# Kernel tuning notes

Measured on AMD Instinct MI355X. Metric: run time of the kernel, lower is better.

## Reference

```python
import jax, jax.numpy as jnp
import numpy as np

D_MODEL = 1024

def setup_inputs() -> dict:
    key = jax.random.key(0)
    kx, kq, kk, kv, ko = jax.random.split(key, 5)
    x = jax.random.normal(kx, (4, 4096, D_MODEL), dtype=jnp.float32)
    w_q = jax.random.normal(kq, (D_MODEL, D_MODEL), dtype=jnp.float32)
    w_k = jax.random.normal(kk, (D_MODEL, D_MODEL), dtype=jnp.float32)
    w_v = jax.random.normal(kv, (D_MODEL, D_MODEL), dtype=jnp.float32)
    w_o = jax.random.normal(ko, (D_MODEL, D_MODEL), dtype=jnp.float32)
    return {"x": x, "w_q": w_q, "w_k": w_k, "w_v": w_v, "w_o": w_o}

def reference(x, w_q, w_k, w_v, w_o):
    # Q/K/V projections: [B,T,D] @ [D,D] -> [B,T,D]
    q = jnp.einsum('btd,de->bte', x, w_q)
    k = jnp.einsum('btd,de->bte', x, w_k)
    v = jnp.einsum('btd,de->bte', x, w_v)
    # Unnormalized attention: scores [B,T,T] (no softmax)
    scores = jnp.einsum('btd,bsd->bts', q, k)
    attn_output = jnp.einsum('bts,bsd->btd', scores, v)
    # Output projection
    output = jnp.einsum('btd,de->bte', attn_output, w_o)
    return output
```

## Files before the change

### kernel.cpp

```cpp
#include <hip/hip_runtime.h>
#include <hip/hip_bf16.h>
#include <stdint.h>

typedef unsigned short u16;
typedef short bf16x8 __attribute__((ext_vector_type(8)));
typedef float f32x4 __attribute__((ext_vector_type(4)));

#define GLOAD16(gp, lp) __builtin_amdgcn_global_load_lds( \
    (const __attribute__((address_space(1))) uint32_t*)(gp), \
    (__attribute__((address_space(3))) uint32_t*)(lp), 16, 0, 0)

#define VMCNT10 do { asm volatile("s_waitcnt vmcnt(10)" ::: "memory"); \
                     __builtin_amdgcn_sched_barrier(0); } while (0)
#define SBAR    do { __builtin_amdgcn_s_barrier(); \
                     __builtin_amdgcn_sched_barrier(0); } while (0)
#define LGKM0   do { asm volatile("s_waitcnt lgkmcnt(0)" ::: "memory"); \
                     __builtin_amdgcn_sched_barrier(0); } while (0)

__device__ __forceinline__ u16 f2bf(float f) {
  union { float f; uint32_t u; } x; x.f = f;
  return (u16)((x.u + 0x7FFFu + ((x.u >> 16) & 1u)) >> 16);
}
__device__ __forceinline__ float bf2f(u16 h) {
  union { uint32_t u; float f; } x; x.u = (uint32_t)h << 16;
  return x.f;
}

__device__ __forceinline__ void xcd_swizzle(int& bx, int& by, int& bz) {
  const int gx = gridDim.x, gy = gridDim.y;
  const int nwg = gx * gy * (int)gridDim.z;
  const int lin = ((int)blockIdx.z * gy + (int)blockIdx.y) * gx + (int)blockIdx.x;
  const int q = nwg >> 3;
  const int wl = (lin & 7) * q + (lin >> 3);
  bz = wl / (gx * gy);
  const int rem = wl - bz * gx * gy;
  by = rem / gx;
  bx = rem - by * gx;
}

__global__ __launch_bounds__(256) void cast_stream(const float* __restrict__ x,
                                                   const float* __restrict__ wq,
                                                   const float* __restrict__ wk,
                                                   const float* __restrict__ wv,
                                                   const float* __restrict__ wo,
                                                   u16* __restrict__ xb,
                                                   u16* __restrict__ WA,
                                                   u16* __restrict__ WBb) {
  __shared__ float tile[64][65];
  const int lin = blockIdx.x;
  const int t = threadIdx.x;
  if (lin < 2048) {
    const float* src = x + (size_t)lin * 8192;
    u16* dst = xb + (size_t)lin * 8192;
#pragma unroll
    for (int i = 0; i < 4; ++i) {
      const int e = i * 2048 + t * 8;
      float4 a = *(const float4*)&src[e];
      float4 b = *(const float4*)&src[e + 4];
      u16 p[8];
      p[0] = f2bf(a.x); p[1] = f2bf(a.y); p[2] = f2bf(a.z); p[3] = f2bf(a.w);
      p[4] = f2bf(b.x); p[5] = f2bf(b.y); p[6] = f2bf(b.z); p[7] = f2bf(b.w);
      *(uint4*)&dst[e] = *(const uint4*)p;
    }
  } else if (lin < 3584) {
    const int e0 = (lin - 2048) * 2048 + t * 8;
    const int w = e0 >> 20;
    const int loc = e0 & 1048575;
    const float* in = w == 0 ? wq : w == 1 ? wk : wv;
    u16* o = w == 0 ? WA : w == 1 ? WBb : WBb + 1048576;
    float4 a = *(const float4*)&in[loc];
    float4 b = *(const float4*)&in[loc + 4];
    u16 p[8];
    p[0] = f2bf(a.x); p[1] = f2bf(a.y); p[2] = f2bf(a.z); p[3] = f2bf(a.w);
    p[4] = f2bf(b.x); p[5] = f2bf(b.y); p[6] = f2bf(b.z); p[7] = f2bf(b.w);
    *(uint4*)&o[loc] = *(const uint4*)p;
  } else {
    const int w2 = lin - 3584;
    const int r0 = (w2 >> 4) * 64, c0 = (w2 & 15) * 64;
    const int lr = t >> 2, lc = (t & 3) * 16;
    const float* src = wo + (size_t)(r0 + lr) * 1024 + c0 + lc;
#pragma unroll
    for (int j = 0; j < 4; ++j) {
      float4 v = *(const float4*)&src[j * 4];
      tile[lr][lc + j * 4 + 0] = v.x;
      tile[lr][lc + j * 4 + 1] = v.y;
      tile[lr][lc + j * 4 + 2] = v.z;
      tile[lr][lc + j * 4 + 3] = v.w;
    }
    __syncthreads();
    u16 tr[16];
#pragma unroll
    for (int j = 0; j < 16; ++j) tr[j] = f2bf(tile[lc + j][lr]);
    u16* dst = WA + 1048576 + (size_t)(c0 + lr) * 1024 + r0 + lc;
    *(uint4*)&dst[0] = *(const uint4*)&tr[0];
    *(uint4*)&dst[8] = *(const uint4*)&tr[8];
  }
}

__global__ __launch_bounds__(256) void transpose_x(const u16* __restrict__ xb,
                                                   u16* __restrict__ xTt) {
  __shared__ u16 ldsT[128][72];
  const int tile = blockIdx.x;
  const int dtile = tile >> 8, tchunk = tile & 255;
  const int t = threadIdx.x;
  const int lr = t >> 2;
  const int dq = (t & 3) * 32;
  const u16* src = xb + (size_t)(tchunk * 64 + lr) * 1024 + dtile * 128 + dq;
#pragma unroll
  for (int i = 0; i < 4; ++i) {
    u16 v[8];
    *(uint4*)v = *(const uint4*)&src[i * 8];
#pragma unroll
    for (int j = 0; j < 8; ++j) ldsT[dq + i * 8 + j][lr] = v[j];
  }
  __syncthreads();
  const int d = t >> 1, seg = (t & 1) * 32;
  u16* dst = xTt + (size_t)tile * 8192 + d * 64 + seg;
#pragma unroll
  for (int i = 0; i < 4; ++i)
    *(uint4*)&dst[i * 8] = *(const uint4*)&ldsT[d][seg + i * 8];
}

__global__ __launch_bounds__(512) void gram_w12(const u16* __restrict__ xTt,
                                                u16* __restrict__ Gp,
                                                const u16* __restrict__ WA,
                                                const u16* __restrict__ WBb,
                                                u16* __restrict__ W12) {
  __shared__ u16 lds[2 * 8192];
  const int lin = blockIdx.x;
  const int wl = (lin & 7) * 88 + (lin >> 3);
  const u16 *Abase, *Bbase;
  u16* Cb;
  int lda, sKt, ldc;
  if (wl < 576) {
    const int z = wl / 36, t5 = wl - z * 36;
    const int b = z >> 2, kc = z & 3;
    int ti = 0;
    while ((ti + 1) * (ti + 2) / 2 <= t5) ++ti;
    const int tj = t5 - ti * (ti + 1) / 2;
    const int tc0 = b * 64 + kc * 16;
    Abase = xTt + (size_t)(ti * 256 + tc0) * 8192;
    Bbase = xTt + (size_t)(tj * 256 + tc0) * 8192;
    lda = 64; sKt = 8192;
    Cb = Gp + ((size_t)z * 36 + t5) * 16384;
    ldc = 128;
  } else {
    const int w = wl - 576;
    const int z2 = w >> 6, tl = w & 63;
    const int by = tl >> 3, bx = tl & 7;
    Abase = WA + (size_t)z2 * 1048576 + (size_t)(by * 128) * 1024;
    Bbase = WBb + (size_t)z2 * 1048576 + (size_t)(bx * 128) * 1024;
    lda = 1024; sKt = 64;
    Cb = W12 + (size_t)z2 * 1048576 + (size_t)(by * 128) * 1024 + bx * 128;
    ldc = 1024;
  }

  const int t = threadIdx.x;
  const int l = t & 63;
  const int wid = t >> 6;
  const int wr = wid >> 2, wc = wid & 3;
  const int lr16 = l & 15, hi = l >> 4;

  f32x4 acc[4][2];
#pragma unroll
  for (int m = 0; m < 4; ++m)
#pragma unroll
    for (int n = 0; n < 2; ++n) acc[m][n] = (f32x4){0.f, 0.f, 0.f, 0.f};

  for (int s = 0; s < 16; ++s) {
    __syncthreads();
    const u16* As = Abase + (size_t)s * sKt;
    const u16* Bs = Bbase + (size_t)s * sKt;
#pragma unroll
    for (int i = 0; i < 2; ++i) {
      int slot = i * 512 + t;
      int row = slot >> 3, cp = slot & 7;
      int clog = cp ^ (row & 7);
      GLOAD16(As + (size_t)row * lda + clog * 8, &lds[slot * 8]);
    }
#pragma unroll
    for (int i = 0; i < 2; ++i) {
      int slot = i * 512 + t;
      int row = slot >> 3, cp = slot & 7;
      int clog = cp ^ (row & 7);
      GLOAD16(Bs + (size_t)row * lda + clog * 8, &lds[8192 + slot * 8]);
    }
    asm volatile("s_waitcnt vmcnt(0)" ::: "memory");
    __syncthreads();
#pragma unroll
    for (int ks = 0; ks < 2; ++ks) {
      bf16x8 af[4], bfr[2];
#pragma unroll
      for (int m = 0; m < 4; ++m) {
        int row = wr * 64 + m * 16 + lr16;
        int p = (ks * 4 + hi) ^ (row & 7);
        af[m] = *(const bf16x8*)&lds[row * 64 + p * 8];
      }
#pragma unroll
      for (int n = 0; n < 2; ++n) {
        int row = wc * 32 + n * 16 + lr16;
        int p = (ks * 4 + hi) ^ (row & 7);
        bfr[n] = *(const bf16x8*)&lds[8192 + row * 64 + p * 8];
      }
#pragma unroll
      for (int m = 0; m < 4; ++m)
#pragma unroll
        for (int n = 0; n < 2; ++n)
          acc[m][n] = __builtin_amdgcn_mfma_f32_16x16x32_bf16(af[m], bfr[n], acc[m][n], 0, 0, 0);
    }
  }

#pragma unroll
  for (int m = 0; m < 4; ++m) {
    int row0 = wr * 64 + m * 16 + hi * 4;
#pragma unroll
    for (int n = 0; n < 2; ++n) {
      int col = wc * 32 + n * 16 + lr16;
      f32x4 v = acc[m][n];
#pragma unroll
      for (int r = 0; r < 4; ++r) Cb[(size_t)(row0 + r) * ldc + col] = f2bf(v[r]);
    }
  }
}

__global__ __launch_bounds__(512) void gemm_bt8(const u16* __restrict__ A,
                                                const u16* __restrict__ B,
                                                u16* __restrict__ C,
                                                int lda, int ldb, int ldc, int K,
                                                size_t sA, size_t sB, size_t sC) {
  __shared__ u16 lds[2 * 8192];
  int bx, by, bz;
  xcd_swizzle(bx, by, bz);
  A += (size_t)bz * sA;
  B += (size_t)bz * sB;
  const int t = threadIdx.x;
  const int l = t & 63;
  const int wid = t >> 6;
  const int wr = wid >> 2, wc = wid & 3;
  const int lr16 = l & 15, hi = l >> 4;
  const int mBase = by * 128;
  const int nBase = bx * 128;

  f32x4 acc[4][2];
#pragma unroll
  for (int m = 0; m < 4; ++m)
#pragma unroll
    for (int n = 0; n < 2; ++n) acc[m][n] = (f32x4){0.f, 0.f, 0.f, 0.f};

  for (int kt = 0; kt < K; kt += 64) {
    __syncthreads();
#pragma unroll
    for (int i = 0; i < 2; ++i) {
      int s = i * 512 + t;
      int row = s >> 3, cp = s & 7;
      int clog = cp ^ (row & 7);
      GLOAD16(A + (size_t)(mBase + row) * lda + kt + clog * 8, &lds[s * 8]);
    }
#pragma unroll
    for (int i = 0; i < 2; ++i) {
      int s = i * 512 + t;
      int row = s >> 3, cp = s & 7;
      int clog = cp ^ (row & 7);
      GLOAD16(B + (size_t)(nBase + row) * ldb + kt + clog * 8, &lds[8192 + s * 8]);
    }
    asm volatile("s_waitcnt vmcnt(0)" ::: "memory");
    __syncthreads();
#pragma unroll
    for (int ks = 0; ks < 2; ++ks) {
      bf16x8 af[4], bfr[2];
#pragma unroll
      for (int m = 0; m < 4; ++m) {
        int row = wr * 64 + m * 16 + lr16;
        int p = (ks * 4 + hi) ^ (row & 7);
        af[m] = *(const bf16x8*)&lds[row * 64 + p * 8];
      }
#pragma unroll
      for (int n = 0; n < 2; ++n) {
        int row = wc * 32 + n * 16 + lr16;
        int p = (ks * 4 + hi) ^ (row & 7);
        bfr[n] = *(const bf16x8*)&lds[8192 + row * 64 + p * 8];
      }
#pragma unroll
      for (int m = 0; m < 4; ++m)
#pragma unroll
        for (int n = 0; n < 2; ++n)
          acc[m][n] = __builtin_amdgcn_mfma_f32_16x16x32_bf16(af[m], bfr[n], acc[m][n], 0, 0, 0);
    }
  }

#pragma unroll
  for (int m = 0; m < 4; ++m) {
    int row0 = mBase + wr * 64 + m * 16 + hi * 4;
#pragma unroll
    for (int n = 0; n < 2; ++n) {
      int col = nBase + wc * 32 + n * 16 + lr16;
      f32x4 v = acc[m][n];
      u16* Cb = C + (size_t)bz * sC;
#pragma unroll
      for (int r = 0; r < 4; ++r) Cb[(size_t)(row0 + r) * ldc + col] = f2bf(v[r]);
    }
  }
}

__global__ __launch_bounds__(256) void reduce_mirror(const u16* __restrict__ Gp,
                                                     u16* __restrict__ G) {
  __shared__ u16 ldsT[128][136];
  const int t5 = blockIdx.x;
  const int b = blockIdx.y;
  int ti = 0;
  while ((ti + 1) * (ti + 2) / 2 <= t5) ++ti;
  const int tj = t5 - ti * (ti + 1) / 2;
  const int tid = threadIdx.x;
  const int rr = tid >> 4, ccc = (tid & 15) * 8;
  u16* Gb = G + (size_t)b * 1048576;
  const size_t ZS = (size_t)36 * 16384;
  const u16* base = Gp + ((size_t)(b * 4) * 36 + t5) * 16384;
#pragma unroll
  for (int i = 0; i < 8; ++i) {
    int row = i * 16 + rr;
    const u16* p = base + row * 128 + ccc;
    u16 a0[8], a1[8], a2[8], a3[8], o[8];
    *(uint4*)a0 = *(const uint4*)&p[0];
    *(uint4*)a1 = *(const uint4*)&p[ZS];
    *(uint4*)a2 = *(const uint4*)&p[2 * ZS];
    *(uint4*)a3 = *(const uint4*)&p[3 * ZS];
#pragma unroll
    for (int j = 0; j < 8; ++j)
      o[j] = f2bf(bf2f(a0[j]) + bf2f(a1[j]) + bf2f(a2[j]) + bf2f(a3[j]));
    *(uint4*)&Gb[(size_t)(ti * 128 + row) * 1024 + tj * 128 + ccc] = *(const uint4*)o;
    *(uint4*)&ldsT[row][ccc] = *(const uint4*)o;
  }
  if (ti != tj) {
    __syncthreads();
#pragma unroll
    for (int i = 0; i < 8; ++i) {
      int row = i * 16 + rr;
      u16 m8[8];
#pragma unroll
      for (int j = 0; j < 8; ++j) m8[j] = ldsT[ccc + j][row];
      *(uint4*)&Gb[(size_t)(tj * 128 + row) * 1024 + ti * 128 + ccc] = *(const uint4*)m8;
    }
  }
}

template <bool F32OUT>
__device__ __forceinline__ void gemm256_core(const u16* __restrict__ A,
                                             const u16* __restrict__ B,
                                             void* __restrict__ C,
                                             int lda, int ldb, int ldc, int K,
                                             int mBase, int nBase, u16* lds) {
  const int t = threadIdx.x;
  const int l = t & 63;
  const int wid = t >> 6;
  const int wr = wid >> 2;
  const int wc = wid & 3;
  const int lr16 = l & 15, hi = l >> 4;
  const int rl0 = t >> 3;
  const int rl1 = rl0 + 64;
  const int cp  = t & 7;
  const int cs  = cp ^ (rl0 & 7);
  const int NT = K >> 6;

  f32x4 acc[8][4];
#pragma unroll
  for (int m = 0; m < 8; ++m)
#pragma unroll
    for (int n = 0; n < 4; ++n) acc[m][n] = (f32x4){0.f, 0.f, 0.f, 0.f};

  auto stage = [&](const u16* g0, int ld, u16* d) {
    GLOAD16(g0 + (size_t)rl0 * ld + cs * 8, d + rl0 * 64 + cp * 8);
    GLOAD16(g0 + (size_t)rl1 * ld + cs * 8, d + rl1 * 64 + cp * 8);
  };
  stage(A + (size_t)mBase * lda,          lda, lds + 0);
  stage(B + (size_t)nBase * ldb,          ldb, lds + 16384);
  stage(B + (size_t)(nBase + 128) * ldb,  ldb, lds + 24576);
  stage(A + (size_t)(mBase + 128) * lda,  lda, lds + 8192);
  stage(B + (size_t)nBase * ldb + 64,         ldb, lds + 32768 + 16384);
  stage(A + (size_t)mBase * lda + 64,         lda, lds + 32768);
  stage(B + (size_t)(nBase + 128) * ldb + 64, ldb, lds + 32768 + 24576);

  bf16x8 af[4][2], b0[2][2], b1[2][2];

  for (int tt = 0; tt < NT; ++tt) {
    const int cur = tt & 1;
    u16* bufA = lds + cur * 32768;
    u16* bufB = bufA + 16384;
    u16* bufN = lds + ((tt + 1) & 1) * 32768;
    int t1 = tt + 1; if (t1 >= NT) t1 -= NT;
    int t2 = tt + 2; if (t2 >= NT) t2 -= NT;
    const int k1 = t1 * 64, k2 = t2 * 64;

    VMCNT10;
    SBAR;
    stage(A + (size_t)(mBase + 128) * lda + k1, lda, bufN + 8192);
#pragma unroll
    for (int mi = 0; mi < 4; ++mi) {
      int row = wr * 64 + mi * 16 + lr16;
#pragma unroll
      for (int kk = 0; kk < 2; ++kk) {
        int p = (kk * 4 + hi) ^ (row & 7);
        af[mi][kk] = *(const bf16x8*)&bufA[row * 64 + p * 8];
      }
    }
#pragma unroll
    for (int ni = 0; ni < 2; ++ni) {
      int row = wc * 32 + ni * 16 + lr16;
#pragma unroll
      for (int kk = 0; kk < 2; ++kk) {
        int p = (kk * 4 + hi) ^ (row & 7);
        b0[ni][kk] = *(const bf16x8*)&bufB[row * 64 + p * 8];
      }
    }
    LGKM0;
    __builtin_amdgcn_s_setprio(1);
#pragma unroll
    for (int kk = 0; kk < 2; ++kk)
#pragma unroll
      for (int mi = 0; mi < 4; ++mi)
#pragma unroll
        for (int ni = 0; ni < 2; ++ni)
          acc[mi][ni] = __builtin_amdgcn_mfma_f32_16x16x32_bf16(af[mi][kk], b0[ni][kk], acc[mi][ni], 0, 0, 0);
    __builtin_amdgcn_s_setprio(0);

    VMCNT10;
    SBAR;
    stage(B + (size_t)nBase * ldb + k2, ldb, bufB);
#pragma unroll
    for (int ni = 0; ni < 2; ++ni) {
      int row = 128 + wc * 32 + ni * 16 + lr16;
#pragma unroll
      for (int kk = 0; kk < 2; ++kk) {
        int p = (kk * 4 + hi) ^ (row & 7);
        b1[ni][kk] = *(const bf16x8*)&bufB[row * 64 + p * 8];
      }
    }
    LGKM0;
    __builtin_amdgcn_s_setprio(1);
#pragma unroll
    for (int kk = 0; kk < 2; ++kk)
#pragma unroll
      for (int mi = 0; mi < 4; ++mi)
#pragma unroll
        for (int ni = 0; ni < 2; ++ni)
          acc[mi][2 + ni] = __builtin_amdgcn_mfma_f32_16x16x32_bf16(af[mi][kk], b1[ni][kk], acc[mi][2 + ni], 0, 0, 0);
    __builtin_amdgcn_s_setprio(0);

    VMCNT10;
    SBAR;
    stage(A + (size_t)mBase * lda + k2, lda, bufA);
#pragma unroll
    for (int mi = 0; mi < 4; ++mi) {
      int row = 128 + wr * 64 + mi * 16 + lr16;
#pragma unroll
      for (int kk = 0; kk < 2; ++kk) {
        int p = (kk * 4 + hi) ^ (row & 7);
        af[mi][kk] = *(const bf16x8*)&bufA[row * 64 + p * 8];
      }
    }
    LGKM0;
    __builtin_amdgcn_s_setprio(1);
#pragma unroll
    for (int kk = 0; kk < 2; ++kk)
#pragma unroll
      for (int mi = 0; mi < 4; ++mi)
#pragma unroll
        for (int ni = 0; ni < 2; ++ni)
          acc[4 + mi][2 + ni] = __builtin_amdgcn_mfma_f32_16x16x32_bf16(af[mi][kk], b1[ni][kk], acc[4 + mi][2 + ni], 0, 0, 0);
    __builtin_amdgcn_s_setprio(0);

    SBAR;
    stage(B + (size_t)(nBase + 128) * ldb + k2, ldb, bufB + 8192);
    __builtin_amdgcn_s_setprio(1);
#pragma unroll
    for (int kk = 0; kk < 2; ++kk)
#pragma unroll
      for (int mi = 0; mi < 4; ++mi)
#pragma unroll
        for (int ni = 0; ni < 2; ++ni)
          acc[4 + mi][ni] = __builtin_amdgcn_mfma_f32_16x16x32_bf16(af[mi][kk], b0[ni][kk], acc[4 + mi][ni], 0, 0, 0);
    __builtin_amdgcn_s_setprio(0);
  }

#pragma unroll
  for (int m = 0; m < 8; ++m) {
    int row0 = mBase + (m >> 2) * 128 + wr * 64 + (m & 3) * 16 + hi * 4;
#pragma unroll
    for (int n = 0; n < 4; ++n) {
      int col = nBase + (n >> 1) * 128 + wc * 32 + (n & 1) * 16 + lr16;
      f32x4 v = acc[m][n];
      if (F32OUT) {
        float* Cf = (float*)C;
#pragma unroll
        for (int r = 0; r < 4; ++r) Cf[(size_t)(row0 + r) * ldc + col] = v[r];
      } else {
        u16* Cb = (u16*)C;
#pragma unroll
        for (int r = 0; r < 4; ++r) Cb[(size_t)(row0 + r) * ldc + col] = f2bf(v[r]);
      }
    }
  }
}

__global__ __launch_bounds__(512) void gemm256_out(const u16* __restrict__ xb,
                                                   const u16* __restrict__ PT,
                                                   float* __restrict__ out) {
  __shared__ u16 lds[65536];
  int bx, by, bz;
  xcd_swizzle(bx, by, bz);
  const u16* Bp = PT + (size_t)(by >> 4) * 1048576;
  gemm256_core<true>(xb, Bp, out, 1024, 1024, 1024, 1024, by * 256, bx * 256, lds);
}

extern "C" void kernel_launch(void* const* d_in, const int* in_sizes, int n_in,
                              void* d_out, int out_size, void* d_ws, size_t ws_size,
                              hipStream_t stream) {
  const float* x  = (const float*)d_in[0];
  const float* wq = (const float*)d_in[1];
  const float* wk = (const float*)d_in[2];
  const float* wv = (const float*)d_in[3];
  const float* wo = (const float*)d_in[4];
  float* out = (float*)d_out;

  u16* ws = (u16*)d_ws;
  const size_t MW = 1048576;
  u16* xb  = ws;
  u16* xTt = ws + 16 * MW;
  u16* WA  = ws + 32 * MW;
  u16* WBb = ws + 34 * MW;
  u16* W12 = ws + 36 * MW;
  u16* G   = ws + 38 * MW;
  u16* S   = ws + 42 * MW;
  u16* PT  = ws + 46 * MW;
  u16* Gp  = ws + 50 * MW;

  cast_stream<<<3840, 256, 0, stream>>>(x, wq, wk, wv, wo, xb, WA, WBb);
  transpose_x<<<2048, 256, 0, stream>>>(xb, xTt);

  gram_w12<<<704, 512, 0, stream>>>(xTt, Gp, WA, WBb, W12);
  reduce_mirror<<<dim3(36, 4), 256, 0, stream>>>(Gp, G);

  gemm_bt8<<<dim3(8, 8, 4), 512, 0, stream>>>(W12 + MW, G, S,
                                              1024, 1024, 1024, 1024,
                                              0, MW, MW);
  gemm_bt8<<<dim3(8, 8, 4), 512, 0, stream>>>(S, W12, PT,
                                              1024, 1024, 1024, 1024,
                                              MW, 0, MW);
  gemm256_out<<<dim3(4, 64), 512, 0, stream>>>(xb, PT, out);
}
```

Baseline: 156.4 us.

## Fuse x cast and transpose into one kernel with weight casts

Merges the fp32-to-bf16 cast of x, the tiled transpose of x and the weight casts into a single 256-block kernel. Each block loads 64 rows of x, writes the bf16 rows and transposes them through a swizzled 144KB LDS buffer. This removes one launch and the re-read of the bf16 x from global memory. In exchange the grid drops to 256 large blocks with heavy LDS use, one block per CU, and the x loads use narrow float2 accesses in a serial 64-iteration loop, which may lower memory-level parallelism.

Measured after the change: 148.2 us. 5.3% less time.

```diff
diff --git a/kernel.cpp b/kernel.cpp
--- a/kernel.cpp
+++ b/kernel.cpp
@@ -38,87 +38,82 @@
   bx = rem - by * gx;
 }
 
-__global__ __launch_bounds__(256) void cast_stream(const float* __restrict__ x,
-                                                   const float* __restrict__ wq,
-                                                   const float* __restrict__ wk,
-                                                   const float* __restrict__ wv,
-                                                   const float* __restrict__ wo,
-                                                   u16* __restrict__ xb,
-                                                   u16* __restrict__ WA,
-                                                   u16* __restrict__ WBb) {
-  __shared__ float tile[64][65];
-  const int lin = blockIdx.x;
+__global__ __launch_bounds__(512) void cast_x_all(const float* __restrict__ x,
+                                                  const float* __restrict__ wq,
+                                                  const float* __restrict__ wk,
+                                                  const float* __restrict__ wv,
+                                                  const float* __restrict__ wo,
+                                                  u16* __restrict__ xb,
+                                                  u16* __restrict__ xTt,
+                                                  u16* __restrict__ WA,
+                                                  u16* __restrict__ WBb) {
+  __shared__ u16 ldsT[73728];
+  const int b = blockIdx.x;
   const int t = threadIdx.x;
-  if (lin < 2048) {
-    const float* src = x + (size_t)lin * 8192;
-    u16* dst = xb + (size_t)lin * 8192;
-#pragma unroll
-    for (int i = 0; i < 4; ++i) {
-      const int e = i * 2048 + t * 8;
-      float4 a = *(const float4*)&src[e];
-      float4 b = *(const float4*)&src[e + 4];
-      u16 p[8];
-      p[0] = f2bf(a.x); p[1] = f2bf(a.y); p[2] = f2bf(a.z); p[3] = f2bf(a.w);
-      p[4] = f2bf(b.x); p[5] = f2bf(b.y); p[6] = f2bf(b.z); p[7] = f2bf(b.w);
-      *(uint4*)&dst[e] = *(const uint4*)p;
-    }
-  } else if (lin < 3584) {
-    const int e0 = (lin - 2048) * 2048 + t * 8;
-    const int w = e0 >> 20;
-    const int loc = e0 & 1048575;
+  const int t0 = b * 64;
+
+  const int fA = (t & 7) << 3;
+  const int d2 = t * 2;
+  const int rowA0 = d2 * 72;
+  const int rowA1 = rowA0 + 72;
+  for (int j = 0; j < 64; ++j) {
+    float2 v = *(const float2*)&x[(size_t)(t0 + j) * 1024 + d2];
+    u16 p0 = f2bf(v.x), p1 = f2bf(v.y);
+    *(uint32_t*)&xb[(size_t)(t0 + j) * 1024 + d2] =
+        (uint32_t)p0 | ((uint32_t)p1 << 16);
+    const int jc = j ^ fA;
+    ldsT[rowA0 + jc] = p0;
+    ldsT[rowA1 + jc] = p1;
+  }
+  __syncthreads();
+
+#pragma unroll
+  for (int k = 0; k < 16; ++k) {
+    const int idx = k * 4096 + t * 8;
+    const int tile = idx >> 13;
+    const int o = idx & 8191;
+    const int dl = o >> 6, c = o & 63;
+    const int d = tile * 128 + dl;
+    const int f = ((dl >> 1) & 7) << 3;
+    uint4 val = *(const uint4*)&ldsT[d * 72 + (c ^ f)];
+    *(uint4*)&xTt[((size_t)(tile * 256 + b)) * 8192 + dl * 64 + c] = val;
+  }
+
+#pragma unroll
+  for (int r = 0; r < 3; ++r) {
+    const int e = b * 12288 + r * 4096 + t * 8;
+    const int w = e >> 20, loc = e & 1048575;
     const float* in = w == 0 ? wq : w == 1 ? wk : wv;
-    u16* o = w == 0 ? WA : w == 1 ? WBb : WBb + 1048576;
+    u16* o2 = w == 0 ? WA : w == 1 ? WBb : WBb + 1048576;
     float4 a = *(const float4*)&in[loc];
-    float4 b = *(const float4*)&in[loc + 4];
+    float4 c4 = *(const float4*)&in[loc + 4];
     u16 p[8];
-    p[0] = f2bf(a.x); p[1] = f2bf(a.y); p[2] = f2bf(a.z); p[3] = f2bf(a.w);
-    p[4] = f2bf(b.x); p[5] = f2bf(b.y); p[6] = f2bf(b.z); p[7] = f2bf(b.w);
-    *(uint4*)&o[loc] = *(const uint4*)p;
-  } else {
-    const int w2 = lin - 3584;
-    const int r0 = (w2 >> 4) * 64, c0 = (w2 & 15) * 64;
-    const int lr = t >> 2, lc = (t & 3) * 16;
+    p[0] = f2bf(a.x);  p[1] = f2bf(a.y);  p[2] = f2bf(a.z);  p[3] = f2bf(a.w);
+    p[4] = f2bf(c4.x); p[5] = f2bf(c4.y); p[6] = f2bf(c4.z); p[7] = f2bf(c4.w);
+    *(uint4*)&o2[loc] = *(const uint4*)p;
+  }
+
+  __syncthreads();
+  float (*tf)[65] = (float(*)[65])ldsT;
+  const int r0 = (b >> 4) * 64, c0 = (b & 15) * 64;
+  const int lr = t >> 3, lc = (t & 7) * 8;
+  {
     const float* src = wo + (size_t)(r0 + lr) * 1024 + c0 + lc;
-#pragma unroll
-    for (int j = 0; j < 4; ++j) {
-      float4 v = *(const float4*)&src[j * 4];
-      tile[lr][lc + j * 4 + 0] = v.x;
-      tile[lr][lc + j * 4 + 1] = v.y;
-      tile[lr][lc + j * 4 + 2] = v.z;
-      tile[lr][lc + j * 4 + 3] = v.w;
-    }
-    __syncthreads();
-    u16 tr[16];
-#pragma unroll
-    for (int j = 0; j < 16; ++j) tr[j] = f2bf(tile[lc + j][lr]);
+    float4 v0 = *(const float4*)&src[0];
+    float4 v1 = *(const float4*)&src[4];
+    tf[lr][lc + 0] = v0.x; tf[lr][lc + 1] = v0.y;
+    tf[lr][lc + 2] = v0.z; tf[lr][lc + 3] = v0.w;
+    tf[lr][lc + 4] = v1.x; tf[lr][lc + 5] = v1.y;
+    tf[lr][lc + 6] = v1.z; tf[lr][lc + 7] = v1.w;
+  }
+  __syncthreads();
+  {
+    u16 tr[8];
+#pragma unroll
+    for (int j = 0; j < 8; ++j) tr[j] = f2bf(tf[lc + j][lr]);
     u16* dst = WA + 1048576 + (size_t)(c0 + lr) * 1024 + r0 + lc;
-    *(uint4*)&dst[0] = *(const uint4*)&tr[0];
-    *(uint4*)&dst[8] = *(const uint4*)&tr[8];
-  }
-}
-
-__global__ __launch_bounds__(256) void transpose_x(const u16* __restrict__ xb,
-                                                   u16* __restrict__ xTt) {
-  __shared__ u16 ldsT[128][72];
-  const int tile = blockIdx.x;
-  const int dtile = tile >> 8, tchunk = tile & 255;
-  const int t = threadIdx.x;
-  const int lr = t >> 2;
-  const int dq = (t & 3) * 32;
-  const u16* src = xb + (size_t)(tchunk * 64 + lr) * 1024 + dtile * 128 + dq;
-#pragma unroll
-  for (int i = 0; i < 4; ++i) {
-    u16 v[8];
-    *(uint4*)v = *(const uint4*)&src[i * 8];
-#pragma unroll
-    for (int j = 0; j < 8; ++j) ldsT[dq + i * 8 + j][lr] = v[j];
-  }
-  __syncthreads();
-  const int d = t >> 1, seg = (t & 1) * 32;
-  u16* dst = xTt + (size_t)tile * 8192 + d * 64 + seg;
-#pragma unroll
-  for (int i = 0; i < 4; ++i)
-    *(uint4*)&dst[i * 8] = *(const uint4*)&ldsT[d][seg + i * 8];
+    *(uint4*)&dst[0] = *(const uint4*)tr;
+  }
 }
 
 __global__ __launch_bounds__(512) void gram_w12(const u16* __restrict__ xTt,
@@ -533,8 +528,7 @@
   u16* PT  = ws + 46 * MW;
   u16* Gp  = ws + 50 * MW;
 
-  cast_stream<<<3840, 256, 0, stream>>>(x, wq, wk, wv, wo, xb, WA, WBb);
-  transpose_x<<<2048, 256, 0, stream>>>(xb, xTt);
+  cast_x_all<<<256, 512, 0, stream>>>(x, wq, wk, wv, wo, xb, xTt, WA, WBb);
 
   gram_w12<<<704, 512, 0, stream>>>(xTt, Gp, WA, WBb, W12);
   reduce_mirror<<<dim3(36, 4), 256, 0, stream>>>(Gp, G);
```
